# Kernel tuning notes

Measured on AMD Instinct MI355X. Metric: run time of the kernel, lower is better.

The kernel has to match this reference:

```python
import jax, jax.numpy as jnp
import numpy as np

NUM_HEADS = 8


def setup_inputs() -> dict:
    key = jax.random.key(0)
    ks = jax.random.split(key, 8)
    b, m, d = 8, 2048, 512
    sc = 1.0 / np.sqrt(d)
    return {
        "x": jax.random.normal(ks[0], (b, m, d), jnp.float32),
        "w_q": jax.random.normal(ks[1], (d, d), jnp.float32) * sc,
        "w_k": jax.random.normal(ks[2], (d, d), jnp.float32) * sc,
        "w_v": jax.random.normal(ks[3], (d, d), jnp.float32) * sc,
        "in_proj_w": jax.random.normal(ks[4], (3 * d, d), jnp.float32) * sc,
        "in_proj_b": jax.random.normal(ks[5], (3 * d,), jnp.float32) * 0.01,
        "out_w": jax.random.normal(ks[6], (d, d), jnp.float32) * sc,
        "out_b": jax.random.normal(ks[7], (d,), jnp.float32) * 0.01,
    }


def _rope_cos_sin(m, d):
    # faithful to source: theta = 10000 ** (-2*(i-1)/d), i = 0..d/2-1
    i = jnp.arange(d // 2, dtype=jnp.float32)
    theta = jnp.power(10000.0, -2.0 * (i - 1.0) / d)
    ang = jnp.arange(m, dtype=jnp.float32)[:, None] * theta  # [m, d/2]
    return jnp.cos(ang), jnp.sin(ang)


def reference(x, w_q, w_k, w_v, in_proj_w, in_proj_b, out_w, out_b):
    b, m, d = x.shape
    h, hd = NUM_HEADS, d // NUM_HEADS
    c, s = _rope_cos_sin(m, d)

    def rot(t):
        # equivalent to t[pos] @ R[pos] with the source's block-rotation matrix
        te = t.reshape(b, m, d // 2, 2)
        e, o = te[..., 0], te[..., 1]
        return jnp.stack([e * c + o * s, -e * s + o * c], axis=-1).reshape(b, m, d)

    q = rot(x @ w_q.T)
    k = rot(x @ w_k.T)
    v = rot(x @ w_v.T)

    # nn.MultiheadAttention's internal in_proj
    wqi, wki, wvi = jnp.split(in_proj_w, 3, axis=0)
    bqi, bki, bvi = jnp.split(in_proj_b, 3, axis=0)
    q = (q @ wqi.T + bqi).reshape(b, m, h, hd)
    k = (k @ wki.T + bki).reshape(b, m, h, hd)
    v = (v @ wvi.T + bvi).reshape(b, m, h, hd)

    scale = 1.0 / jnp.sqrt(jnp.asarray(hd, x.dtype))
    scores = jnp.einsum("bqhd,bkhd->bhqk", q, k) * scale
    causal = jnp.triu(jnp.ones((m, m), bool), k=1)
    scores = jnp.where(causal, jnp.finfo(x.dtype).min, scores)
    attn = jax.nn.softmax(scores, axis=-1)
    ctx = jnp.einsum("bhqk,bkhd->bqhd", attn, v).reshape(b, m, d)
    return ctx @ out_w.T + out_b
```

## Files before the change

kernel.cpp:

```cpp
#include <hip/hip_runtime.h>
#include <hip/hip_bf16.h>

typedef __attribute__((ext_vector_type(8))) short short8;
typedef __attribute__((ext_vector_type(4))) short short4v;
typedef __attribute__((ext_vector_type(4))) float f32x4;

__device__ __forceinline__ float bf2f(unsigned short u) {
    union { unsigned int i; float f; } v; v.i = ((unsigned int)u) << 16; return v.f;
}
__device__ __forceinline__ unsigned short f2bf(float f) {
    union { float f; unsigned int i; } v; v.f = f;
    unsigned int r = v.i + 0x7fffu + ((v.i >> 16) & 1u);
    return (unsigned short)(r >> 16);
}

#define GLDS16(g, l) __builtin_amdgcn_global_load_lds( \
    (const __attribute__((address_space(1))) unsigned int*)(g), \
    (__attribute__((address_space(3))) unsigned int*)(l), 16, 0, 0)

__global__ __launch_bounds__(256) void cvt_one(
    const float* __restrict__ in, unsigned short* __restrict__ out, int nchunk)
{
    int i = blockIdx.x * 256 + threadIdx.x;
    if (i >= nchunk) return;
    f32x4 a = *(const f32x4*)&in[(size_t)i * 8];
    f32x4 b = *(const f32x4*)&in[(size_t)i * 8 + 4];
    short8 o;
    o[0] = (short)f2bf(a[0]); o[1] = (short)f2bf(a[1]);
    o[2] = (short)f2bf(a[2]); o[3] = (short)f2bf(a[3]);
    o[4] = (short)f2bf(b[0]); o[5] = (short)f2bf(b[1]);
    o[6] = (short)f2bf(b[2]); o[7] = (short)f2bf(b[3]);
    *(short8*)&out[(size_t)i * 8] = o;
}

template<int HAS_BIAS, int OUT>
__global__ __launch_bounds__(256) void gemm_bt(
    const unsigned short* __restrict__ A, const unsigned short* __restrict__ B,
    const float* __restrict__ bias, void* __restrict__ Cp,
    int M, int N, int K)
{
    __shared__ __align__(16) short As[128 * 64];
    __shared__ __align__(16) short Bs[128 * 64];
    const int tid  = threadIdx.x;
    const int lane = tid & 63;
    const int wave = tid >> 6;
    const int wr = wave >> 1, wc = wave & 1;
    const int lo = lane & 15, hi = lane >> 4;
    const int rowBase = blockIdx.y * 128;
    const int colBase = blockIdx.x * 128;

    f32x4 acc[4][4] = {};

    for (int k0 = 0; k0 < K; k0 += 64) {
        const unsigned short* Ab = A + (size_t)rowBase * K + k0;
        const unsigned short* Bb = B + (size_t)colBase * K + k0;
        #pragma unroll
        for (int p = 0; p < 4; ++p) {
            int o = p * 256 + tid;
            GLDS16(&Ab[(size_t)(o >> 3) * K + (o & 7) * 8], &As[o * 8]);
        }
        #pragma unroll
        for (int p = 0; p < 4; ++p) {
            int o = p * 256 + tid;
            GLDS16(&Bb[(size_t)(o >> 3) * K + (o & 7) * 8], &Bs[o * 8]);
        }
        __syncthreads();
        #pragma unroll
        for (int s = 0; s < 2; ++s) {
            short8 a[4], b[4];
            #pragma unroll
            for (int i = 0; i < 4; ++i)
                a[i] = *(const short8*)&As[(wr * 64 + i * 16 + lo) * 64 + s * 32 + hi * 8];
            #pragma unroll
            for (int j = 0; j < 4; ++j)
                b[j] = *(const short8*)&Bs[(wc * 64 + j * 16 + lo) * 64 + s * 32 + hi * 8];
            #pragma unroll
            for (int i = 0; i < 4; ++i)
                #pragma unroll
                for (int j = 0; j < 4; ++j)
                    acc[i][j] = __builtin_amdgcn_mfma_f32_16x16x32_bf16(a[i], b[j], acc[i][j], 0, 0, 0);
        }
        __syncthreads();
    }

    #pragma unroll
    for (int i = 0; i < 4; ++i) {
        int rowA = rowBase + wr * 64 + i * 16 + hi * 4;
        #pragma unroll
        for (int j = 0; j < 4; ++j) {
            int col = colBase + wc * 64 + j * 16 + lo;
            float bv = HAS_BIAS ? bias[col] : 0.0f;
            if (OUT == 2) {
                short4v sv;
                #pragma unroll
                for (int r = 0; r < 4; ++r) sv[r] = (short)f2bf(acc[i][j][r] + bv);
                size_t idx = (((size_t)(rowA >> 11) * 8 + (col >> 6)) * 64 + (col & 63)) * 2048
                             + (rowA & 2047);
                *(short4v*)&((unsigned short*)Cp)[idx] = sv;
            } else {
                #pragma unroll
                for (int r = 0; r < 4; ++r) {
                    float v = acc[i][j][r] + bv;
                    if (OUT == 1) ((float*)Cp)[(size_t)(rowA + r) * N + col] = v;
                    else          ((unsigned short*)Cp)[(size_t)(rowA + r) * N + col] = f2bf(v);
                }
            }
        }
    }
}

__global__ __launch_bounds__(256) void rope_kernel(unsigned short* __restrict__ T)
{
    int gid = blockIdx.x * 256 + threadIdx.x;
    int row = gid >> 6;
    int seg = (gid & 63) * 8;
    int pos = row & 2047;
    short8 v = *(short8*)&T[(size_t)row * 512 + seg];
    const float THC = -0.05190512648261308f;
    #pragma unroll
    for (int p = 0; p < 4; ++p) {
        int i = (seg >> 1) + p;
        float theta = exp2f(THC * ((float)i - 1.0f));
        float ang = (float)pos * theta;
        float sn, cs;
        sincosf(ang, &sn, &cs);
        float e = bf2f((unsigned short)v[2 * p]);
        float o = bf2f((unsigned short)v[2 * p + 1]);
        v[2 * p]     = (short)f2bf(e * cs + o * sn);
        v[2 * p + 1] = (short)f2bf(-e * sn + o * cs);
    }
    *(short8*)&T[(size_t)row * 512 + seg] = v;
}


__device__ __forceinline__ void attn_step(
    int kt, int NT, int qrow, int lo, int hi,
    const short* __restrict__ KsB, const short* __restrict__ VsB,
    short* __restrict__ Pw,
    short8 (&aq)[2], f32x4 (&o_acc)[4],
    float (&m_i)[4], float (&l_i)[4])
{
    const int swz = (lo & 7) << 3;

    f32x4 sa[4] = {};
    #pragma unroll
    for (int s = 0; s < 2; ++s) {
        short8 bk[4];
        #pragma unroll
        for (int n = 0; n < 4; ++n)
            bk[n] = *(const short8*)&KsB[(n * 16 + lo) * 64 + ((s * 32 + hi * 8) ^ swz)];
        #pragma unroll
        for (int n = 0; n < 4; ++n)
            sa[n] = __builtin_amdgcn_mfma_f32_16x16x32_bf16(aq[s], bk[n], sa[n], 0, 0, 0);
    }

    const bool need_mask = (kt == NT - 1);
    float sv[4][4];
    #pragma unroll
    for (int n = 0; n < 4; ++n) {
        int key = kt * 64 + n * 16 + lo;
        #pragma unroll
        for (int r = 0; r < 4; ++r) {
            float x = sa[n][r] * 0.125f;
            if (need_mask) {
                int qr = qrow + hi * 4 + r;
                if (key > qr) x = -1e30f;
            }
            sv[n][r] = x;
        }
    }

    float alpha[4];
    #pragma unroll
    for (int r = 0; r < 4; ++r) {
        float x = fmaxf(fmaxf(sv[0][r], sv[1][r]), fmaxf(sv[2][r], sv[3][r]));
        #pragma unroll
        for (int off = 1; off < 16; off <<= 1) x = fmaxf(x, __shfl_xor(x, off));
        float mn = fmaxf(m_i[r], x);
        alpha[r] = __expf(m_i[r] - mn);
        m_i[r] = mn;
    }
    #pragma unroll
    for (int n = 0; n < 4; ++n)
        #pragma unroll
        for (int r = 0; r < 4; ++r)
            sv[n][r] = __expf(sv[n][r] - m_i[r]);

    #pragma unroll
    for (int r = 0; r < 4; ++r) {
        float x = sv[0][r] + sv[1][r] + sv[2][r] + sv[3][r];
        #pragma unroll
        for (int off = 1; off < 16; off <<= 1) x += __shfl_xor(x, off);
        l_i[r] = l_i[r] * alpha[r] + x;
    }
    #pragma unroll
    for (int t = 0; t < 4; ++t)
        #pragma unroll
        for (int r = 0; r < 4; ++r)
            o_acc[t][r] *= alpha[r];

    #pragma unroll
    for (int n = 0; n < 4; ++n)
        #pragma unroll
        for (int r = 0; r < 4; ++r)
            Pw[(hi * 4 + r) * 72 + n * 16 + lo] = (short)f2bf(sv[n][r]);

    #pragma unroll
    for (int s = 0; s < 2; ++s) {
        short8 ap = *(const short8*)&Pw[lo * 72 + s * 32 + hi * 8];
        #pragma unroll
        for (int t = 0; t < 4; ++t) {
            short8 bv = *(const short8*)&VsB[(t * 16 + lo) * 64 + ((s * 32 + hi * 8) ^ swz)];
            o_acc[t] = __builtin_amdgcn_mfma_f32_16x16x32_bf16(ap, bv, o_acc[t], 0, 0, 0);
        }
    }
}

#define STG_LOAD(kt, KR0, KR1, VR0, VR1) { \
    int rr = tid >> 3, cc = (tid & 7) * 8; \
    KR0 = *(const short8*)&Kp[(rowQ + (size_t)((kt) * 64 + rr)) * 512 + colBase + cc]; \
    KR1 = *(const short8*)&Kp[(rowQ + (size_t)((kt) * 64 + rr + 32)) * 512 + colBase + cc]; \
    VR0 = *(const short8*)&Vh[(size_t)rr * 2048 + (kt) * 64 + cc]; \
    VR1 = *(const short8*)&Vh[(size_t)(rr + 32) * 2048 + (kt) * 64 + cc]; }

#define STG_WRITE(BUF, KR0, KR1, VR0, VR1) { \
    int rr = tid >> 3; \
    int sw = ((tid & 7) * 8) ^ ((rr & 7) << 3); \
    *(short8*)&Ks[BUF][rr * 64 + sw] = KR0; \
    *(short8*)&Ks[BUF][(rr + 32) * 64 + sw] = KR1; \
    *(short8*)&Vs[BUF][rr * 64 + sw] = VR0; \
    *(short8*)&Vs[BUF][(rr + 32) * 64 + sw] = VR1; }

__global__ __launch_bounds__(256, 3) void attn_kernel(
    const unsigned short* __restrict__ Q, const unsigned short* __restrict__ Kp,
    const unsigned short* __restrict__ Vt, unsigned short* __restrict__ O)
{
    const int tid = threadIdx.x, lane = tid & 63, wave = tid >> 6;
    const int lo = lane & 15, hi = lane >> 4;
    const int bh = blockIdx.x;
    const int qb = 31 - blockIdx.y;
    const int bb = bh >> 3, hh = bh & 7;
    const int NT = qb + 1;

    __shared__ __align__(16) short Ks[2][64 * 64];
    __shared__ __align__(16) short Vs[2][64 * 64];
    __shared__ __align__(16) short P[4][16 * 72];
    short* Pw = P[wave];

    const size_t rowQ = (size_t)bb * 2048;
    const int colBase = hh * 64;
    const unsigned short* Vh = Vt + (size_t)bh * 64 * 2048;
    const int qrow = qb * 64 + wave * 16;

    short8 aq[2];
    #pragma unroll
    for (int s = 0; s < 2; ++s)
        aq[s] = *(const short8*)&Q[(rowQ + qrow + lo) * 512 + colBase + s * 32 + hi * 8];

    f32x4 o_acc[4] = {};
    float m_i[4], l_i[4];
    #pragma unroll
    for (int r = 0; r < 4; ++r) { m_i[r] = -1e30f; l_i[r] = 0.0f; }

    short8 ka0, ka1, va0, va1;
    short8 kb0, kb1, vb0, vb1;

    STG_LOAD(0, ka0, ka1, va0, va1);
    STG_WRITE(0, ka0, ka1, va0, va1);
    if (1 < NT) STG_LOAD(1, kb0, kb1, vb0, vb1);
    __syncthreads();

    for (int kt = 0; kt < NT; ) {
        if (kt + 1 < NT) STG_WRITE(1, kb0, kb1, vb0, vb1);
        if (kt + 2 < NT) STG_LOAD(kt + 2, ka0, ka1, va0, va1);
        attn_step(kt, NT, qrow, lo, hi, Ks[0], Vs[0], Pw, aq, o_acc, m_i, l_i);
        __syncthreads();
        ++kt;
        if (kt >= NT) break;
        if (kt + 1 < NT) STG_WRITE(0, ka0, ka1, va0, va1);
        if (kt + 2 < NT) STG_LOAD(kt + 2, kb0, kb1, vb0, vb1);
        attn_step(kt, NT, qrow, lo, hi, Ks[1], Vs[1], Pw, aq, o_acc, m_i, l_i);
        __syncthreads();
        ++kt;
    }

    #pragma unroll
    for (int t = 0; t < 4; ++t)
        #pragma unroll
        for (int r = 0; r < 4; ++r) {
            float v = o_acc[t][r] / l_i[r];
            O[(rowQ + qrow + hi * 4 + r) * 512 + colBase + t * 16 + lo] = f2bf(v);
        }
}

extern "C" void kernel_launch(void* const* d_in, const int* in_sizes, int n_in,
                              void* d_out, int out_size, void* d_ws, size_t ws_size,
                              hipStream_t stream)
{
    (void)in_sizes; (void)n_in; (void)out_size; (void)ws_size;
    const float* x   = (const float*)d_in[0];
    const float* w_q = (const float*)d_in[1];
    const float* w_k = (const float*)d_in[2];
    const float* w_v = (const float*)d_in[3];
    const float* ipw = (const float*)d_in[4];
    const float* ipb = (const float*)d_in[5];
    const float* ow  = (const float*)d_in[6];
    const float* ob  = (const float*)d_in[7];

    const int M = 16384, D = 512;
    const size_t SZ = (size_t)M * D;
    unsigned short* xb   = (unsigned short*)d_ws;
    unsigned short* wqb  = xb + SZ;
    unsigned short* wkb  = wqb + 262144;
    unsigned short* wvb  = wkb + 262144;
    unsigned short* ipwb = wvb + 262144;
    unsigned short* owb  = ipwb + 786432;
    unsigned short* T    = owb + 262144;
    unsigned short* Kb   = T + 3 * SZ;
    unsigned short* Vt   = Kb + SZ;
    unsigned short* Qb   = xb;
    unsigned short* Cb   = T;

    dim3 blk(256);
    dim3 gg(D / 128, M / 128);

    cvt_one<<<dim3((int)(SZ / 8 / 256)), blk, 0, stream>>>(x, xb, (int)(SZ / 8));
    cvt_one<<<dim3(128), blk, 0, stream>>>(w_q, wqb, 32768);
    cvt_one<<<dim3(128), blk, 0, stream>>>(w_k, wkb, 32768);
    cvt_one<<<dim3(128), blk, 0, stream>>>(w_v, wvb, 32768);
    cvt_one<<<dim3(384), blk, 0, stream>>>(ipw, ipwb, 98304);
    cvt_one<<<dim3(128), blk, 0, stream>>>(ow, owb, 32768);

    gemm_bt<0, 0><<<gg, blk, 0, stream>>>(xb, wqb, nullptr, T,          M, D, D);
    gemm_bt<0, 0><<<gg, blk, 0, stream>>>(xb, wkb, nullptr, T + SZ,     M, D, D);
    gemm_bt<0, 0><<<gg, blk, 0, stream>>>(xb, wvb, nullptr, T + 2 * SZ, M, D, D);

    rope_kernel<<<dim3(3 * M * 64 / 256), blk, 0, stream>>>(T);

    gemm_bt<1, 0><<<gg, blk, 0, stream>>>(T,          ipwb,          ipb,        Qb, M, D, D);
    gemm_bt<1, 0><<<gg, blk, 0, stream>>>(T + SZ,     ipwb + 262144, ipb + 512,  Kb, M, D, D);
    gemm_bt<1, 2><<<gg, blk, 0, stream>>>(T + 2 * SZ, ipwb + 524288, ipb + 1024, Vt, M, D, D);

    attn_kernel<<<dim3(64, 32), blk, 0, stream>>>(Qb, Kb, Vt, Cb);

    gemm_bt<1, 1><<<gg, blk, 0, stream>>>(Cb, owb, ob, (float*)d_out, M, D, D);
}
```

Before: 357.5 us.

## Batch projection GEMMs, precompute RoPE table, and merge weight conversions

The three Q/K/V projections become one GEMM with N=1536 writing an interleaved buffer, and the three in-projection GEMMs become one launch over blockIdx.z. The five weight conversion launches are merged into one. RoPE cos/sin values now come from a precomputed table instead of per-element sincos. The 0.125 attention scale is folded into Q at load time, and a library bf16 conversion replaces the manual rounding. Together these cut launch count and transcendental work, at the cost of an extra table kernel and a slightly different rounding path for the scaled Q.

```diff
diff --git a/kernel.cpp b/kernel.cpp
--- a/kernel.cpp
+++ b/kernel.cpp
@@ -8,10 +8,10 @@
 __device__ __forceinline__ float bf2f(unsigned short u) {
     union { unsigned int i; float f; } v; v.i = ((unsigned int)u) << 16; return v.f;
 }
-__device__ __forceinline__ unsigned short f2bf(float f) {
-    union { float f; unsigned int i; } v; v.f = f;
-    unsigned int r = v.i + 0x7fffu + ((v.i >> 16) & 1u);
-    return (unsigned short)(r >> 16);
+__device__ __forceinline__ unsigned short f2bfh(float f) {
+    union { __hip_bfloat16 h; unsigned short u; } c;
+    c.h = __float2bfloat16(f);
+    return c.u;
 }
 
 #define GLDS16(g, l) __builtin_amdgcn_global_load_lds( \
@@ -26,38 +26,64 @@
     f32x4 a = *(const f32x4*)&in[(size_t)i * 8];
     f32x4 b = *(const f32x4*)&in[(size_t)i * 8 + 4];
     short8 o;
-    o[0] = (short)f2bf(a[0]); o[1] = (short)f2bf(a[1]);
-    o[2] = (short)f2bf(a[2]); o[3] = (short)f2bf(a[3]);
-    o[4] = (short)f2bf(b[0]); o[5] = (short)f2bf(b[1]);
-    o[6] = (short)f2bf(b[2]); o[7] = (short)f2bf(b[3]);
+    o[0] = (short)f2bfh(a[0]); o[1] = (short)f2bfh(a[1]);
+    o[2] = (short)f2bfh(a[2]); o[3] = (short)f2bfh(a[3]);
+    o[4] = (short)f2bfh(b[0]); o[5] = (short)f2bfh(b[1]);
+    o[6] = (short)f2bfh(b[2]); o[7] = (short)f2bfh(b[3]);
     *(short8*)&out[(size_t)i * 8] = o;
 }
 
-template<int HAS_BIAS, int OUT>
-__global__ __launch_bounds__(256) void gemm_bt(
-    const unsigned short* __restrict__ A, const unsigned short* __restrict__ B,
-    const float* __restrict__ bias, void* __restrict__ Cp,
-    int M, int N, int K)
-{
-    __shared__ __align__(16) short As[128 * 64];
-    __shared__ __align__(16) short Bs[128 * 64];
-    const int tid  = threadIdx.x;
-    const int lane = tid & 63;
-    const int wave = tid >> 6;
+__global__ __launch_bounds__(256) void cvt_w(
+    const float* __restrict__ wq, const float* __restrict__ wk, const float* __restrict__ wv,
+    const float* __restrict__ ipw, const float* __restrict__ ow,
+    unsigned short* __restrict__ wqb, unsigned short* __restrict__ ipwb,
+    unsigned short* __restrict__ owb)
+{
+    int z = blockIdx.y;
+    const float* src;
+    unsigned short* dst;
+    if (z < 3)      { src = (z == 0 ? wq : z == 1 ? wk : wv); dst = wqb + (size_t)z * 262144; }
+    else if (z < 6) { src = ipw + (size_t)(z - 3) * 262144;   dst = ipwb + (size_t)(z - 3) * 262144; }
+    else            { src = ow;                                dst = owb; }
+    int i = blockIdx.x * 256 + threadIdx.x;
+    f32x4 a = *(const f32x4*)&src[(size_t)i * 8];
+    f32x4 b = *(const f32x4*)&src[(size_t)i * 8 + 4];
+    short8 o;
+    o[0] = (short)f2bfh(a[0]); o[1] = (short)f2bfh(a[1]);
+    o[2] = (short)f2bfh(a[2]); o[3] = (short)f2bfh(a[3]);
+    o[4] = (short)f2bfh(b[0]); o[5] = (short)f2bfh(b[1]);
+    o[6] = (short)f2bfh(b[2]); o[7] = (short)f2bfh(b[3]);
+    *(short8*)&dst[(size_t)i * 8] = o;
+}
+
+__global__ __launch_bounds__(256) void rope_table(float* __restrict__ ct, float* __restrict__ st)
+{
+    int i = threadIdx.x;
+    int pos = blockIdx.x;
+    const float THC = -0.05190512648261308f;
+    float theta = exp2f(THC * ((float)i - 1.0f));
+    float ang = (float)pos * theta;
+    float sn, cs;
+    sincosf(ang, &sn, &cs);
+    ct[pos * 256 + i] = cs;
+    st[pos * 256 + i] = sn;
+}
+
+__device__ __forceinline__ void gemm_core(
+    const unsigned short* __restrict__ A, int lda,
+    const unsigned short* __restrict__ B, int K,
+    int rowBase, int colBase, int tid, int lane, int wave,
+    short* As, short* Bs, f32x4 (&acc)[4][4])
+{
     const int wr = wave >> 1, wc = wave & 1;
     const int lo = lane & 15, hi = lane >> 4;
-    const int rowBase = blockIdx.y * 128;
-    const int colBase = blockIdx.x * 128;
-
-    f32x4 acc[4][4] = {};
-
     for (int k0 = 0; k0 < K; k0 += 64) {
-        const unsigned short* Ab = A + (size_t)rowBase * K + k0;
+        const unsigned short* Ab = A + (size_t)rowBase * lda + k0;
         const unsigned short* Bb = B + (size_t)colBase * K + k0;
         #pragma unroll
         for (int p = 0; p < 4; ++p) {
             int o = p * 256 + tid;
-            GLDS16(&Ab[(size_t)(o >> 3) * K + (o & 7) * 8], &As[o * 8]);
+            GLDS16(&Ab[(size_t)(o >> 3) * lda + (o & 7) * 8], &As[o * 8]);
         }
         #pragma unroll
         for (int p = 0; p < 4; ++p) {
@@ -82,6 +108,24 @@
         }
         __syncthreads();
     }
+}
+
+template<int HAS_BIAS, int OUT>
+__global__ __launch_bounds__(256) void gemm_bt(
+    const unsigned short* __restrict__ A, int lda, const unsigned short* __restrict__ B,
+    const float* __restrict__ bias, void* __restrict__ Cp,
+    int M, int N, int K)
+{
+    __shared__ __align__(16) short As[128 * 64];
+    __shared__ __align__(16) short Bs[128 * 64];
+    const int tid = threadIdx.x, lane = tid & 63, wave = tid >> 6;
+    const int wr = wave >> 1, wc = wave & 1;
+    const int lo = lane & 15, hi = lane >> 4;
+    const int rowBase = blockIdx.y * 128;
+    const int colBase = blockIdx.x * 128;
+
+    f32x4 acc[4][4] = {};
+    gemm_core(A, lda, B, K, rowBase, colBase, tid, lane, wave, As, Bs, acc);
 
     #pragma unroll
     for (int i = 0; i < 4; ++i) {
@@ -90,46 +134,81 @@
         for (int j = 0; j < 4; ++j) {
             int col = colBase + wc * 64 + j * 16 + lo;
             float bv = HAS_BIAS ? bias[col] : 0.0f;
-            if (OUT == 2) {
+            #pragma unroll
+            for (int r = 0; r < 4; ++r) {
+                float v = acc[i][j][r] + bv;
+                if (OUT == 1) ((float*)Cp)[(size_t)(rowA + r) * N + col] = v;
+                else          ((unsigned short*)Cp)[(size_t)(rowA + r) * N + col] = f2bfh(v);
+            }
+        }
+    }
+}
+
+__global__ __launch_bounds__(256) void gemm_inproj(
+    const unsigned short* __restrict__ T, const unsigned short* __restrict__ ipwb,
+    const float* __restrict__ ipb,
+    unsigned short* __restrict__ Qb, unsigned short* __restrict__ Kb,
+    unsigned short* __restrict__ Vt)
+{
+    __shared__ __align__(16) short As[128 * 64];
+    __shared__ __align__(16) short Bs[128 * 64];
+    const int tid = threadIdx.x, lane = tid & 63, wave = tid >> 6;
+    const int wr = wave >> 1, wc = wave & 1;
+    const int lo = lane & 15, hi = lane >> 4;
+    const int rowBase = blockIdx.y * 128;
+    const int colBase = blockIdx.x * 128;
+    const int z = blockIdx.z;
+
+    const unsigned short* A = T + z * 512;
+    const unsigned short* B = ipwb + (size_t)z * 262144;
+    const float* bias = ipb + z * 512;
+
+    f32x4 acc[4][4] = {};
+    gemm_core(A, 1536, B, 512, rowBase, colBase, tid, lane, wave, As, Bs, acc);
+
+    unsigned short* Crm = (z == 0) ? Qb : Kb;
+    #pragma unroll
+    for (int i = 0; i < 4; ++i) {
+        int rowA = rowBase + wr * 64 + i * 16 + hi * 4;
+        #pragma unroll
+        for (int j = 0; j < 4; ++j) {
+            int col = colBase + wc * 64 + j * 16 + lo;
+            float bv = bias[col];
+            if (z == 2) {
                 short4v sv;
                 #pragma unroll
-                for (int r = 0; r < 4; ++r) sv[r] = (short)f2bf(acc[i][j][r] + bv);
+                for (int r = 0; r < 4; ++r) sv[r] = (short)f2bfh(acc[i][j][r] + bv);
                 size_t idx = (((size_t)(rowA >> 11) * 8 + (col >> 6)) * 64 + (col & 63)) * 2048
                              + (rowA & 2047);
-                *(short4v*)&((unsigned short*)Cp)[idx] = sv;
+                *(short4v*)&Vt[idx] = sv;
             } else {
                 #pragma unroll
-                for (int r = 0; r < 4; ++r) {
-                    float v = acc[i][j][r] + bv;
-                    if (OUT == 1) ((float*)Cp)[(size_t)(rowA + r) * N + col] = v;
-                    else          ((unsigned short*)Cp)[(size_t)(rowA + r) * N + col] = f2bf(v);
-                }
+                for (int r = 0; r < 4; ++r)
+                    Crm[(size_t)(rowA + r) * 512 + col] = f2bfh(acc[i][j][r] + bv);
             }
         }
     }
 }
 
-__global__ __launch_bounds__(256) void rope_kernel(unsigned short* __restrict__ T)
-{
-    int gid = blockIdx.x * 256 + threadIdx.x;
-    int row = gid >> 6;
-    int seg = (gid & 63) * 8;
+__global__ __launch_bounds__(192) void rope_kernel(
+    unsigned short* __restrict__ T,
+    const float* __restrict__ ct, const float* __restrict__ st)
+{
+    int row = blockIdx.x;
+    int c0 = threadIdx.x * 8;
     int pos = row & 2047;
-    short8 v = *(short8*)&T[(size_t)row * 512 + seg];
-    const float THC = -0.05190512648261308f;
+    int i0 = (c0 & 511) >> 1;
+    short8 v = *(short8*)&T[(size_t)row * 1536 + c0];
+    f32x4 cs = *(const f32x4*)&ct[pos * 256 + i0];
+    f32x4 sn = *(const f32x4*)&st[pos * 256 + i0];
     #pragma unroll
     for (int p = 0; p < 4; ++p) {
-        int i = (seg >> 1) + p;
-        float theta = exp2f(THC * ((float)i - 1.0f));
-        float ang = (float)pos * theta;
-        float sn, cs;
-        sincosf(ang, &sn, &cs);
         float e = bf2f((unsigned short)v[2 * p]);
         float o = bf2f((unsigned short)v[2 * p + 1]);
-        v[2 * p]     = (short)f2bf(e * cs + o * sn);
-        v[2 * p + 1] = (short)f2bf(-e * sn + o * cs);
-    }
-    *(short8*)&T[(size_t)row * 512 + seg] = v;
+        v[2 * p]     = (short)f2bfh(e * cs[p] + o * sn[p]);
+        v[2 * p + 1] = (short)f2bfh(-e * sn[p] + o * cs[p]);
+    }
+    *(short8*)&T[(size_t)row * 1536 + c0] = v;
 }
 
 
@@ -161,7 +240,7 @@
         int key = kt * 64 + n * 16 + lo;
         #pragma unroll
         for (int r = 0; r < 4; ++r) {
-            float x = sa[n][r] * 0.125f;
+            float x = sa[n][r];
             if (need_mask) {
                 int qr = qrow + hi * 4 + r;
                 if (key > qr) x = -1e30f;
@@ -203,7 +282,7 @@
     for (int n = 0; n < 4; ++n)
         #pragma unroll
         for (int r = 0; r < 4; ++r)
-            Pw[(hi * 4 + r) * 72 + n * 16 + lo] = (short)f2bf(sv[n][r]);
+            Pw[(hi * 4 + r) * 72 + n * 16 + lo] = (short)f2bfh(sv[n][r]);
 
     #pragma unroll
     for (int s = 0; s < 2; ++s) {
@@ -254,8 +333,12 @@
 
     short8 aq[2];
     #pragma unroll
-    for (int s = 0; s < 2; ++s)
+    for (int s = 0; s < 2; ++s) {
         aq[s] = *(const short8*)&Q[(rowQ + qrow + lo) * 512 + colBase + s * 32 + hi * 8];
+        #pragma unroll
+        for (int e = 0; e < 8; ++e)
+            aq[s][e] = (short)f2bfh(bf2f((unsigned short)aq[s][e]) * 0.125f);
+    }
 
     f32x4 o_acc[4] = {};
     float m_i[4], l_i[4];
@@ -289,7 +372,7 @@
         #pragma unroll
         for (int r = 0; r < 4; ++r) {
             float v = o_acc[t][r] / l_i[r];
-            O[(rowQ + qrow + hi * 4 + r) * 512 + colBase + t * 16 + lo] = f2bf(v);
+            O[(rowQ + qrow + hi * 4 + r) * 512 + colBase + t * 16 + lo] = f2bfh(v);
         }
 }
 
@@ -307,41 +390,33 @@
     const float* ow  = (const float*)d_in[6];
     const float* ob  = (const float*)d_in[7];
 
-    const int M = 16384, D = 512;
-    const size_t SZ = (size_t)M * D;
+    const int M = 16384;
+    const size_t SZ = (size_t)M * 512;
     unsigned short* xb   = (unsigned short*)d_ws;
     unsigned short* wqb  = xb + SZ;
-    unsigned short* wkb  = wqb + 262144;
-    unsigned short* wvb  = wkb + 262144;
-    unsigned short* ipwb = wvb + 262144;
+    unsigned short* ipwb = wqb + 786432;
     unsigned short* owb  = ipwb + 786432;
     unsigned short* T    = owb + 262144;
-    unsigned short* Kb   = T + 3 * SZ;
+    unsigned short* Kb   = T + (size_t)M * 1536;
     unsigned short* Vt   = Kb + SZ;
+    float* ct = (float*)(Vt + SZ);
+    float* st = ct + 524288;
     unsigned short* Qb   = xb;
     unsigned short* Cb   = T;
 
     dim3 blk(256);
-    dim3 gg(D / 128, M / 128);
 
     cvt_one<<<dim3((int)(SZ / 8 / 256)), blk, 0, stream>>>(x, xb, (int)(SZ / 8));
-    cvt_one<<<dim3(128), blk, 0, stream>>>(w_q, wqb, 32768);
-    cvt_one<<<dim3(128), blk, 0, stream>>>(w_k, wkb, 32768);
-    cvt_one<<<dim3(128), blk, 0, stream>>>(w_v, wvb, 32768);
-    cvt_one<<<dim3(384), blk, 0, stream>>>(ipw, ipwb, 98304);
-    cvt_one<<<dim3(128), blk, 0, stream>>>(ow, owb, 32768);
-
-    gemm_bt<0, 0><<<gg, blk, 0, stream>>>(xb, wqb, nullptr, T,          M, D, D);
-    gemm_bt<0, 0><<<gg, blk, 0, stream>>>(xb, wkb, nullptr, T + SZ,     M, D, D);
-    gemm_bt<0, 0><<<gg, blk, 0, stream>>>(xb, wvb, nullptr, T + 2 * SZ, M, D, D);
-
-    rope_kernel<<<dim3(3 * M * 64 / 256), blk, 0, stream>>>(T);
-
-    gemm_bt<1, 0><<<gg, blk, 0, stream>>>(T,          ipwb,          ipb,        Qb, M, D, D);
-    gemm_bt<1, 0><<<gg, blk, 0, stream>>>(T + SZ,     ipwb + 262144, ipb + 512,  Kb, M, D, D);
-    gemm_bt<1, 2><<<gg, blk, 0, stream>>>(T + 2 * SZ, ipwb + 524288, ipb + 1024, Vt, M, D, D);
+    cvt_w<<<dim3(128, 7), blk, 0, stream>>>(w_q, w_k, w_v, ipw, ow, wqb, ipwb, owb);
+    rope_table<<<dim3(2048), blk, 0, stream>>>(ct, st);
+
+    gemm_bt<0, 0><<<dim3(12, 128), blk, 0, stream>>>(xb, 512, wqb, nullptr, T, M, 1536, 512);
+
+    rope_kernel<<<dim3(M), dim3(192), 0, stream>>>(T, ct, st);
+
+    gemm_inproj<<<dim3(4, 128, 3), blk, 0, stream>>>(T, ipwb, ipb, Qb, Kb, Vt);
 
     attn_kernel<<<dim3(64, 32), blk, 0, stream>>>(Qb, Kb, Vt, Cb);
 
-    gemm_bt<1, 1><<<gg, blk, 0, stream>>>(Cb, owb, ob, (float*)d_out, M, D, D);
-}
+    gemm_bt<1, 1><<<dim3(4, 128), blk, 0, stream>>>(Cb, 512, owb, ob, (float*)d_out, M, 512, 512);
+}
```

Result: faster. 338.7 us (-5.2%).
